# Kernel optimization log

Measured on AMD Instinct MI355X. Metric: run time of the kernel, lower is better.

The kernel has to match this reference:

```python
import jax, jax.numpy as jnp
import numpy as np

D_MODEL = 1024
BATCH = 8
SEQ = 2048
LN_EPS = 1e-5


def setup_inputs() -> dict:
    key = jax.random.key(0)
    ks = jax.random.split(key, 8)
    scale = 0.1 / np.sqrt(D_MODEL)
    x = jax.random.normal(ks[0], (BATCH, SEQ, D_MODEL), dtype=jnp.float32)
    return {
        "x": x,
        "ln_w": jnp.ones((D_MODEL,), jnp.float32),
        "ln_b": jnp.zeros((D_MODEL,), jnp.float32),
        # layer_idx=0, n_layers=4 -> ratio_1 = 1.0 (init), perturb slightly for a non-trivial mix
        "tmk": jnp.ones((D_MODEL,), jnp.float32) * 0.9,
        "tmv": jnp.ones((D_MODEL,), jnp.float32) * 0.9,
        "tmr": jnp.ones((D_MODEL,), jnp.float32) * 0.9,
        "decay_w": jnp.full((D_MODEL,), -0.5, jnp.float32)
        + 0.1 * jax.random.normal(ks[1], (D_MODEL,), jnp.float32),
        "Wk": scale * jax.random.normal(ks[2], (D_MODEL, D_MODEL), jnp.float32),
        "Wv": scale * jax.random.normal(ks[3], (D_MODEL, D_MODEL), jnp.float32),
        "Wr": scale * jax.random.normal(ks[4], (D_MODEL, D_MODEL), jnp.float32),
        "Wo": scale * jax.random.normal(ks[5], (D_MODEL, D_MODEL), jnp.float32),
    }


def _layernorm(z, w, b):
    m = jnp.mean(z, axis=-1, keepdims=True)
    v = jnp.mean(jnp.square(z - m), axis=-1, keepdims=True)
    return (z - m) * jax.lax.rsqrt(v + LN_EPS) * w + b


def reference(x, ln_w, ln_b, tmk, tmv, tmr, decay_w, Wk, Wv, Wr, Wo):
    # x: (B, T, D)
    xn = _layernorm(x, ln_w, ln_b)
    # prev_x at t=0 is zeros (not LN of zeros), afterwards LN(x_{t-1})
    prev = jnp.pad(xn[:, :-1, :], ((0, 0), (1, 0), (0, 0)))
    xk = xn * tmk + prev * (1.0 - tmk)
    xv = xn * tmv + prev * (1.0 - tmv)
    xr = xn * tmr + prev * (1.0 - tmr)
    k = jnp.einsum("btd,ed->bte", xk, Wk)
    v = jnp.einsum("btd,ed->bte", xv, Wv)
    r = jax.nn.sigmoid(jnp.einsum("btd,ed->bte", xr, Wr))
    decay = jax.nn.sigmoid(decay_w)  # (D,)

    kv = (k * v).swapaxes(0, 1)  # (T, B, D) time-major for scan

    def step(S, kv_t):
        S_new = decay * S + kv_t
        return S_new, S_new

    S0 = jnp.zeros((x.shape[0], x.shape[2]), x.dtype)
    final_S, S_seq = jax.lax.scan(step, S0, kv)
    S_seq = S_seq.swapaxes(0, 1)  # (B, T, D)

    out = x + r * jnp.einsum("btd,ed->bte", S_seq, Wo)
    return out, final_S, S_seq
```

## Files before the change

kernel.cpp:

```cpp
#include <hip/hip_runtime.h>
#include <cstdint>

#define D_MODEL 1024
#define SEQ 2048
#define BATCH 8
#define M_TOTAL (BATCH*SEQ)
#define NC 64
#define CL (SEQ/NC)

typedef float f32x4 __attribute__((ext_vector_type(4)));
typedef short bf16x8 __attribute__((ext_vector_type(8)));
typedef unsigned short u16x4 __attribute__((ext_vector_type(4)));

__device__ __forceinline__ float b2f(unsigned short s){
  union { float f; unsigned u; } z; z.u = ((unsigned)s) << 16; return z.f;
}
__device__ __forceinline__ unsigned short f2b(float f){
  union { float f; unsigned u; } z; z.f = f;
  unsigned u = z.u;
  u += 0x7fffu + ((u >> 16) & 1u);
  return (unsigned short)(u >> 16);
}
__device__ __forceinline__ float sigmoidf_(float v){
  return 1.0f / (1.0f + __expf(-v));
}
__device__ __forceinline__ void gld_lds16(const void* g, void* l){
  __builtin_amdgcn_global_load_lds((const __attribute__((address_space(1))) unsigned int*)g,
                                   (__attribute__((address_space(3))) unsigned int*)l,
                                   16, 0, 0);
}

__device__ __forceinline__ void swz256(int bid, int& m0, int& n0){
  int xcd = bid & 7;
  int loc = bid >> 3;
  int wg  = xcd*32 + loc;
  m0 = (wg >> 2) * 256;
  n0 = (wg & 3) * 256;
}

__global__ __launch_bounds__(256) void wconv_kernel(const float* __restrict__ W0, const float* __restrict__ W1,
                                                    const float* __restrict__ W2, const float* __restrict__ W3,
                                                    unsigned short* __restrict__ WC){
  int mat = blockIdx.y;
  const float* src = (mat==0) ? W0 : (mat==1) ? W1 : (mat==2) ? W2 : W3;
  size_t i = ((size_t)blockIdx.x*256 + threadIdx.x)*4;
  f32x4 v = *(const f32x4*)(src + i);
  u16x4 o; o[0]=f2b(v[0]); o[1]=f2b(v[1]); o[2]=f2b(v[2]); o[3]=f2b(v[3]);
  *(u16x4*)(WC + (size_t)mat*1048576 + i) = o;
}

__global__ __launch_bounds__(256) void lnmix_kernel(const float* __restrict__ x,
                                                    const float* __restrict__ lnw, const float* __restrict__ lnb,
                                                    const float* __restrict__ tmk, const float* __restrict__ tmv,
                                                    const float* __restrict__ tmr,
                                                    unsigned short* __restrict__ XK, unsigned short* __restrict__ XV,
                                                    unsigned short* __restrict__ XR){
  int m = blockIdx.x;
  int tid = threadIdx.x;
  bool first = (m & (SEQ-1)) == 0;
  size_t base = (size_t)m*D_MODEL + tid*4;
  f32x4 xc = *(const f32x4*)(x + base);
  f32x4 xp = {0.f,0.f,0.f,0.f};
  if (!first) xp = *(const f32x4*)(x + base - D_MODEL);

  float c1 = xc[0]+xc[1]+xc[2]+xc[3];
  float c2 = xc[0]*xc[0]+xc[1]*xc[1]+xc[2]*xc[2]+xc[3]*xc[3];
  float p1 = xp[0]+xp[1]+xp[2]+xp[3];
  float p2 = xp[0]*xp[0]+xp[1]*xp[1]+xp[2]*xp[2]+xp[3]*xp[3];
  #pragma unroll
  for (int off = 32; off > 0; off >>= 1){
    c1 += __shfl_xor(c1, off); c2 += __shfl_xor(c2, off);
    p1 += __shfl_xor(p1, off); p2 += __shfl_xor(p2, off);
  }
  __shared__ float rc1[4], rc2[4], rp1[4], rp2[4];
  int w = tid >> 6, lane = tid & 63;
  if (lane == 0){ rc1[w]=c1; rc2[w]=c2; rp1[w]=p1; rp2[w]=p2; }
  __syncthreads();
  c1 = rc1[0]+rc1[1]+rc1[2]+rc1[3];
  c2 = rc2[0]+rc2[1]+rc2[2]+rc2[3];
  p1 = rp1[0]+rp1[1]+rp1[2]+rp1[3];
  p2 = rp2[0]+rp2[1]+rp2[2]+rp2[3];
  float mC = c1*(1.0f/1024.0f), vC = c2*(1.0f/1024.0f)-mC*mC, rC = rsqrtf(vC+1e-5f);
  float mP = p1*(1.0f/1024.0f), vP = p2*(1.0f/1024.0f)-mP*mP, rP = rsqrtf(vP+1e-5f);

  f32x4 wv = *(const f32x4*)(lnw + tid*4);
  f32x4 bv = *(const f32x4*)(lnb + tid*4);
  f32x4 k4 = *(const f32x4*)(tmk + tid*4);
  f32x4 v4 = *(const f32x4*)(tmv + tid*4);
  f32x4 r4 = *(const f32x4*)(tmr + tid*4);
  u16x4 ok, ov, orr;
  #pragma unroll
  for (int j=0;j<4;j++){
    float nc = (xc[j]-mC)*rC*wv[j] + bv[j];
    float np = first ? 0.f : (xp[j]-mP)*rP*wv[j] + bv[j];
    ok[j]  = f2b(np + k4[j]*(nc-np));
    ov[j]  = f2b(np + v4[j]*(nc-np));
    orr[j] = f2b(np + r4[j]*(nc-np));
  }
  *(u16x4*)(XK + base) = ok;
  *(u16x4*)(XV + base) = ov;
  *(u16x4*)(XR + base) = orr;
}

__device__ __forceinline__ void gemm256_core(const unsigned short* __restrict__ A,
                                             const unsigned short* __restrict__ W,
                                             int m0, int n0, int tid,
                                             unsigned short* As, unsigned short* Bs,
                                             f32x4 (&acc)[8][4]){
  int wid = tid >> 6, lane = tid & 63;
  int wm = wid >> 2, wn = wid & 3;
  int fr = lane & 15, fg = lane >> 4;

  int offAg[4], offBg[4], offL[4];
  #pragma unroll
  for (int it = 0; it < 4; ++it){
    int chunk = it*512 + tid;
    int row = chunk >> 3;
    int cg = (chunk & 7) ^ (row & 7);
    offAg[it] = (m0+row)*D_MODEL + cg*8;
    offBg[it] = (n0+row)*D_MODEL + cg*8;
    offL[it]  = chunk*8;
  }

  #define STAGE256(bsel, kt) { \
    _Pragma("unroll") \
    for (int it = 0; it < 4; ++it){ \
      gld_lds16(A + offAg[it] + (kt)*64, &As[(bsel)*16384 + offL[it]]); \
      gld_lds16(W + offBg[it] + (kt)*64, &Bs[(bsel)*16384 + offL[it]]); \
    } }

  STAGE256(0, 0);
  for (int kt = 0; kt < 16; ++kt){
    int cur = kt & 1;
    asm volatile("s_waitcnt vmcnt(0)" ::: "memory");
    __builtin_amdgcn_s_barrier();
    if (kt < 15) STAGE256(cur^1, kt+1);
    const unsigned short* Ab = &As[cur*16384];
    const unsigned short* Bb = &Bs[cur*16384];
    #pragma unroll
    for (int ks = 0; ks < 2; ++ks){
      bf16x8 a[8], b[4];
      #pragma unroll
      for (int mi=0; mi<8; ++mi){
        int r = wm*128 + mi*16 + fr;
        a[mi] = *(const bf16x8*)(&Ab[r*64 + (((ks*4+fg) ^ (r&7))<<3)]);
      }
      #pragma unroll
      for (int ni=0; ni<4; ++ni){
        int r = wn*64 + ni*16 + fr;
        b[ni] = *(const bf16x8*)(&Bb[r*64 + (((ks*4+fg) ^ (r&7))<<3)]);
      }
      __builtin_amdgcn_s_setprio(1);
      #pragma unroll
      for (int mi=0; mi<8; ++mi)
        #pragma unroll
        for (int ni=0; ni<4; ++ni)
          acc[mi][ni] = __builtin_amdgcn_mfma_f32_16x16x32_bf16(a[mi], b[ni], acc[mi][ni], 0, 0, 0);
      __builtin_amdgcn_s_setprio(0);
      __builtin_amdgcn_s_barrier();
    }
  }
  #undef STAGE256
}

__global__ __launch_bounds__(512) void gemm_mix3_kernel(const unsigned short* __restrict__ XK,
                                                        const unsigned short* __restrict__ XV,
                                                        const unsigned short* __restrict__ XR,
                                                        const unsigned short* __restrict__ WC,
                                                        unsigned short* __restrict__ KB,
                                                        unsigned short* __restrict__ VB,
                                                        unsigned short* __restrict__ RB){
  __shared__ alignas(16) unsigned short As[2*16384];
  __shared__ alignas(16) unsigned short Bs[2*16384];
  int m0, n0; swz256(blockIdx.x, m0, n0);
  int z = blockIdx.z;
  int tid = threadIdx.x;
  const unsigned short* A = (z==0) ? XK : (z==1) ? XV : XR;
  const unsigned short* W = WC + (size_t)z*1048576;
  unsigned short* O       = (z==0) ? KB : (z==1) ? VB : RB;

  f32x4 acc[8][4];
  #pragma unroll
  for (int i=0;i<8;i++)
    #pragma unroll
    for (int j=0;j<4;j++){ acc[i][j][0]=0.f; acc[i][j][1]=0.f; acc[i][j][2]=0.f; acc[i][j][3]=0.f; }

  gemm256_core(A, W, m0, n0, tid, As, Bs, acc);

  int wid = tid >> 6, lane = tid & 63;
  int wm = wid >> 2, wn = wid & 3;
  int fr = lane & 15, fg = lane >> 4;
  #pragma unroll
  for (int mi=0; mi<8; ++mi){
    #pragma unroll
    for (int ni=0; ni<4; ++ni){
      int c = n0 + wn*64 + ni*16 + fr;
      #pragma unroll
      for (int j=0; j<4; ++j){
        int r = m0 + wm*128 + mi*16 + fg*4 + j;
        size_t idx = (size_t)r*D_MODEL + c;
        float val = acc[mi][ni][j];
        if (z == 2) val = sigmoidf_(val);
        O[idx] = f2b(val);
      }
    }
  }
}

__global__ __launch_bounds__(512) void gemm_out_kernel(const unsigned short* __restrict__ Sb,
                                                       const unsigned short* __restrict__ Wo,
                                                       const float* __restrict__ x,
                                                       const unsigned short* __restrict__ RB,
                                                       float* __restrict__ out){
  __shared__ alignas(16) unsigned short As[2*16384];
  __shared__ alignas(16) unsigned short Bs[2*16384];
  int m0, n0; swz256(blockIdx.x, m0, n0);
  int tid = threadIdx.x;

  f32x4 acc[8][4];
  #pragma unroll
  for (int i=0;i<8;i++)
    #pragma unroll
    for (int j=0;j<4;j++){ acc[i][j][0]=0.f; acc[i][j][1]=0.f; acc[i][j][2]=0.f; acc[i][j][3]=0.f; }

  gemm256_core(Sb, Wo, m0, n0, tid, As, Bs, acc);

  int wid = tid >> 6, lane = tid & 63;
  int wm = wid >> 2, wn = wid & 3;
  int fr = lane & 15, fg = lane >> 4;
  #pragma unroll
  for (int mi=0; mi<8; ++mi){
    #pragma unroll
    for (int ni=0; ni<4; ++ni){
      int c = n0 + wn*64 + ni*16 + fr;
      #pragma unroll
      for (int j=0; j<4; ++j){
        int r = m0 + wm*128 + mi*16 + fg*4 + j;
        size_t idx = (size_t)r*D_MODEL + c;
        float rr = b2f(RB[idx]);
        out[idx] = x[idx] + rr * acc[mi][ni][j];
      }
    }
  }
}

__global__ __launch_bounds__(256) void scan_p1_kernel(const unsigned short* __restrict__ kb,
                                                      const unsigned short* __restrict__ vb,
                                                      const float* __restrict__ dw,
                                                      float* __restrict__ carr){
  int bc = blockIdx.x;
  int b = bc >> 6, c = bc & (NC-1);
  int d0 = threadIdx.x * 4;
  float dx = sigmoidf_(dw[d0+0]);
  float dy = sigmoidf_(dw[d0+1]);
  float dz = sigmoidf_(dw[d0+2]);
  float dwv = sigmoidf_(dw[d0+3]);
  float Sx=0.f, Sy=0.f, Sz=0.f, Sw=0.f;
  size_t base = ((size_t)(b*SEQ + c*CL))*D_MODEL + d0;
  for (int i=0;i<CL;i++){
    u16x4 k4 = *(const u16x4*)(kb + base);
    u16x4 v4 = *(const u16x4*)(vb + base);
    Sx = dx*Sx + b2f(k4[0])*b2f(v4[0]);
    Sy = dy*Sy + b2f(k4[1])*b2f(v4[1]);
    Sz = dz*Sz + b2f(k4[2])*b2f(v4[2]);
    Sw = dwv*Sw + b2f(k4[3])*b2f(v4[3]);
    base += D_MODEL;
  }
  f32x4 o; o[0]=Sx; o[1]=Sy; o[2]=Sz; o[3]=Sw;
  *(f32x4*)(carr + (size_t)bc*D_MODEL + d0) = o;
}

__global__ __launch_bounds__(256) void scan_p2_kernel(const float* __restrict__ dw, float* __restrict__ carr){
  int gid = blockIdx.x*256 + threadIdx.x;
  int b = gid >> 10, d = gid & (D_MODEL-1);
  float dec = sigmoidf_(dw[d]);
  float dL = dec;
  #pragma unroll
  for (int i=0;i<5;i++) dL *= dL;
  float S = 0.f;
  for (int c=0;c<NC;c++){
    size_t idx = ((size_t)(b*NC + c))*D_MODEL + d;
    float cr = carr[idx];
    carr[idx] = S;
    S = dL*S + cr;
  }
}

__global__ __launch_bounds__(256) void scan_p3_kernel(const unsigned short* __restrict__ kb,
                                                      unsigned short* vsb,
                                                      const float* __restrict__ dw,
                                                      const float* __restrict__ cin,
                                                      float* __restrict__ sseq,
                                                      float* __restrict__ finalS){
  int bc = blockIdx.x;
  int b = bc >> 6, c = bc & (NC-1);
  int d0 = threadIdx.x * 4;
  float dx = sigmoidf_(dw[d0+0]);
  float dy = sigmoidf_(dw[d0+1]);
  float dz = sigmoidf_(dw[d0+2]);
  float dwv = sigmoidf_(dw[d0+3]);
  f32x4 S = *(const f32x4*)(cin + (size_t)bc*D_MODEL + d0);
  size_t base = ((size_t)(b*SEQ + c*CL))*D_MODEL + d0;
  for (int i=0;i<CL;i++){
    u16x4 k4 = *(const u16x4*)(kb + base);
    u16x4 v4 = *(const u16x4*)(vsb + base);
    S[0] = dx*S[0] + b2f(k4[0])*b2f(v4[0]);
    S[1] = dy*S[1] + b2f(k4[1])*b2f(v4[1]);
    S[2] = dz*S[2] + b2f(k4[2])*b2f(v4[2]);
    S[3] = dwv*S[3] + b2f(k4[3])*b2f(v4[3]);
    *(f32x4*)(sseq + base) = S;
    u16x4 s4; s4[0]=f2b(S[0]); s4[1]=f2b(S[1]); s4[2]=f2b(S[2]); s4[3]=f2b(S[3]);
    *(u16x4*)(vsb + base) = s4;
    base += D_MODEL;
  }
  if (c == NC-1)
    *(f32x4*)(finalS + (size_t)b*D_MODEL + d0) = S;
}

extern "C" void kernel_launch(void* const* d_in, const int* in_sizes, int n_in,
                              void* d_out, int out_size, void* d_ws, size_t ws_size,
                              hipStream_t stream){
  const float* x   = (const float*)d_in[0];
  const float* lnw = (const float*)d_in[1];
  const float* lnb = (const float*)d_in[2];
  const float* tmk = (const float*)d_in[3];
  const float* tmv = (const float*)d_in[4];
  const float* tmr = (const float*)d_in[5];
  const float* dw  = (const float*)d_in[6];
  const float* Wk  = (const float*)d_in[7];
  const float* Wv  = (const float*)d_in[8];
  const float* Wr  = (const float*)d_in[9];
  const float* Wo  = (const float*)d_in[10];

  float* out    = (float*)d_out;
  float* finalS = out + (size_t)M_TOTAL*D_MODEL;
  float* sseq   = finalS + (size_t)BATCH*D_MODEL;

  unsigned short* XK = (unsigned short*)d_out;
  unsigned short* XV = (unsigned short*)((char*)d_out + 33554432);
  unsigned short* XR = (unsigned short*)sseq;

  char* w = (char*)d_ws;
  unsigned short* WC   = (unsigned short*)(w + 0);
  unsigned short* VSB  = (unsigned short*)(w + 8388608);
  unsigned short* KB   = (unsigned short*)(w + 41943040);
  unsigned short* RB   = (unsigned short*)(w + 75497472);
  float*          CARR = (float*)(w + 109051904);

  wconv_kernel<<<dim3(1024,4), 256, 0, stream>>>(Wk, Wv, Wr, Wo, WC);
  lnmix_kernel<<<M_TOTAL, 256, 0, stream>>>(x, lnw, lnb, tmk, tmv, tmr, XK, XV, XR);

  gemm_mix3_kernel<<<dim3(256,1,3), 512, 0, stream>>>(XK, XV, XR, WC, KB, VSB, RB);

  scan_p1_kernel<<<BATCH*NC, 256, 0, stream>>>(KB, VSB, dw, CARR);
  scan_p2_kernel<<<32, 256, 0, stream>>>(dw, CARR);
  scan_p3_kernel<<<BATCH*NC, 256, 0, stream>>>(KB, VSB, dw, CARR, sseq, finalS);

  gemm_out_kernel<<<256, 512, 0, stream>>>(VSB, WC + (size_t)3*1048576, x, RB, out);
}
```

Measured before the change: 287.8 us.

## Use 256x128 GEMM tiles with triple-buffered LDS and deeper prefetch

Shrinks the GEMM tile from 256x256 to 256x128, which doubles the grid to 512 blocks per matrix (1536 for the fused k/v/r launch), and updates the XCD swizzle to match. The K loop moves from double to triple buffering with a prefetch distance of two. It waits with a partial vmcnt and uses one barrier per iteration instead of two. The aim is more blocks to fill the CUs, fewer accumulator registers, and more load latency hidden. The cost is more LDS (144KB per block), lower arithmetic intensity per tile, and more A re-reads.

```diff
diff --git a/kernel.cpp b/kernel.cpp
--- a/kernel.cpp
+++ b/kernel.cpp
@@ -30,12 +30,12 @@
                                    16, 0, 0);
 }
 
-__device__ __forceinline__ void swz256(int bid, int& m0, int& n0){
+__device__ __forceinline__ void swz_mn(int bid, int& m0, int& n0){
   int xcd = bid & 7;
   int loc = bid >> 3;
-  int wg  = xcd*32 + loc;
-  m0 = (wg >> 2) * 256;
-  n0 = (wg & 3) * 256;
+  int wg  = xcd*64 + loc;
+  m0 = (wg >> 3) * 256;
+  n0 = (wg & 7) * 128;
 }
 
 __global__ __launch_bounds__(256) void wconv_kernel(const float* __restrict__ W0, const float* __restrict__ W1,
@@ -106,61 +106,85 @@
                                              const unsigned short* __restrict__ W,
                                              int m0, int n0, int tid,
                                              unsigned short* As, unsigned short* Bs,
-                                             f32x4 (&acc)[8][4]){
+                                             f32x4 (&acc)[8][2]){
   int wid = tid >> 6, lane = tid & 63;
   int wm = wid >> 2, wn = wid & 3;
   int fr = lane & 15, fg = lane >> 4;
 
-  int offAg[4], offBg[4], offL[4];
+  int offAg[4], offBg[2], offLA[4], offLB[2];
   #pragma unroll
   for (int it = 0; it < 4; ++it){
     int chunk = it*512 + tid;
     int row = chunk >> 3;
     int cg = (chunk & 7) ^ (row & 7);
     offAg[it] = (m0+row)*D_MODEL + cg*8;
+    offLA[it] = chunk*8;
+  }
+  #pragma unroll
+  for (int it = 0; it < 2; ++it){
+    int chunk = it*512 + tid;
+    int row = chunk >> 3;
+    int cg = (chunk & 7) ^ (row & 7);
     offBg[it] = (n0+row)*D_MODEL + cg*8;
-    offL[it]  = chunk*8;
-  }
-
-  #define STAGE256(bsel, kt) { \
+    offLB[it] = chunk*8;
+  }
+
+  #define STAGE(bsel, kt) { \
     _Pragma("unroll") \
-    for (int it = 0; it < 4; ++it){ \
-      gld_lds16(A + offAg[it] + (kt)*64, &As[(bsel)*16384 + offL[it]]); \
-      gld_lds16(W + offBg[it] + (kt)*64, &Bs[(bsel)*16384 + offL[it]]); \
-    } }
-
-  STAGE256(0, 0);
-  for (int kt = 0; kt < 16; ++kt){
-    int cur = kt & 1;
-    asm volatile("s_waitcnt vmcnt(0)" ::: "memory");
+    for (int it = 0; it < 4; ++it) \
+      gld_lds16(A + offAg[it] + (kt)*64, &As[(bsel)*16384 + offLA[it]]); \
+    _Pragma("unroll") \
+    for (int it = 0; it < 2; ++it) \
+      gld_lds16(W + offBg[it] + (kt)*64, &Bs[(bsel)*8192 + offLB[it]]); \
+  }
+
+  #define COMPUTE(bsel) { \
+    const unsigned short* Ab = &As[(bsel)*16384]; \
+    const unsigned short* Bb = &Bs[(bsel)*8192]; \
+    _Pragma("unroll") \
+    for (int ks = 0; ks < 2; ++ks){ \
+      bf16x8 a[8], b[2]; \
+      _Pragma("unroll") \
+      for (int mi=0; mi<8; ++mi){ \
+        int r = wm*128 + mi*16 + fr; \
+        a[mi] = *(const bf16x8*)(&Ab[r*64 + (((ks*4+fg) ^ (r&7))<<3)]); \
+      } \
+      _Pragma("unroll") \
+      for (int ni=0; ni<2; ++ni){ \
+        int r = wn*32 + ni*16 + fr; \
+        b[ni] = *(const bf16x8*)(&Bb[r*64 + (((ks*4+fg) ^ (r&7))<<3)]); \
+      } \
+      __builtin_amdgcn_s_setprio(1); \
+      _Pragma("unroll") \
+      for (int mi=0; mi<8; ++mi) \
+        _Pragma("unroll") \
+        for (int ni=0; ni<2; ++ni) \
+          acc[mi][ni] = __builtin_amdgcn_mfma_f32_16x16x32_bf16(a[mi], b[ni], acc[mi][ni], 0, 0, 0); \
+      __builtin_amdgcn_s_setprio(0); \
+    } \
+  }
+
+  STAGE(0, 0);
+  STAGE(1, 1);
+  int cur = 0;
+  #pragma unroll 1
+  for (int kt = 0; kt < 15; ++kt){
+    asm volatile("s_waitcnt vmcnt(6)" ::: "memory");
     __builtin_amdgcn_s_barrier();
-    if (kt < 15) STAGE256(cur^1, kt+1);
-    const unsigned short* Ab = &As[cur*16384];
-    const unsigned short* Bb = &Bs[cur*16384];
-    #pragma unroll
-    for (int ks = 0; ks < 2; ++ks){
-      bf16x8 a[8], b[4];
-      #pragma unroll
-      for (int mi=0; mi<8; ++mi){
-        int r = wm*128 + mi*16 + fr;
-        a[mi] = *(const bf16x8*)(&Ab[r*64 + (((ks*4+fg) ^ (r&7))<<3)]);
-      }
-      #pragma unroll
-      for (int ni=0; ni<4; ++ni){
-        int r = wn*64 + ni*16 + fr;
-        b[ni] = *(const bf16x8*)(&Bb[r*64 + (((ks*4+fg) ^ (r&7))<<3)]);
-      }
-      __builtin_amdgcn_s_setprio(1);
-      #pragma unroll
-      for (int mi=0; mi<8; ++mi)
-        #pragma unroll
-        for (int ni=0; ni<4; ++ni)
-          acc[mi][ni] = __builtin_amdgcn_mfma_f32_16x16x32_bf16(a[mi], b[ni], acc[mi][ni], 0, 0, 0);
-      __builtin_amdgcn_s_setprio(0);
-      __builtin_amdgcn_s_barrier();
+    asm volatile("" ::: "memory");
+    if (kt < 14){
+      int nb = cur + 2; if (nb >= 3) nb -= 3;
+      STAGE(nb, kt+2);
     }
-  }
-  #undef STAGE256
+    COMPUTE(cur);
+    cur = (cur == 2) ? 0 : cur + 1;
+  }
+  asm volatile("s_waitcnt vmcnt(0)" ::: "memory");
+  __builtin_amdgcn_s_barrier();
+  asm volatile("" ::: "memory");
+  COMPUTE(cur);
+  #undef STAGE
+  #undef COMPUTE
 }
 
 __global__ __launch_bounds__(512) void gemm_mix3_kernel(const unsigned short* __restrict__ XK,
@@ -170,20 +194,20 @@
                                                         unsigned short* __restrict__ KB,
                                                         unsigned short* __restrict__ VB,
                                                         unsigned short* __restrict__ RB){
-  __shared__ alignas(16) unsigned short As[2*16384];
-  __shared__ alignas(16) unsigned short Bs[2*16384];
-  int m0, n0; swz256(blockIdx.x, m0, n0);
+  __shared__ alignas(16) unsigned short As[3*16384];
+  __shared__ alignas(16) unsigned short Bs[3*8192];
+  int m0, n0; swz_mn(blockIdx.x, m0, n0);
   int z = blockIdx.z;
   int tid = threadIdx.x;
   const unsigned short* A = (z==0) ? XK : (z==1) ? XV : XR;
   const unsigned short* W = WC + (size_t)z*1048576;
   unsigned short* O       = (z==0) ? KB : (z==1) ? VB : RB;
 
-  f32x4 acc[8][4];
+  f32x4 acc[8][2];
   #pragma unroll
   for (int i=0;i<8;i++)
     #pragma unroll
-    for (int j=0;j<4;j++){ acc[i][j][0]=0.f; acc[i][j][1]=0.f; acc[i][j][2]=0.f; acc[i][j][3]=0.f; }
+    for (int j=0;j<2;j++){ acc[i][j][0]=0.f; acc[i][j][1]=0.f; acc[i][j][2]=0.f; acc[i][j][3]=0.f; }
 
   gemm256_core(A, W, m0, n0, tid, As, Bs, acc);
 
@@ -193,8 +217,8 @@
   #pragma unroll
   for (int mi=0; mi<8; ++mi){
     #pragma unroll
-    for (int ni=0; ni<4; ++ni){
-      int c = n0 + wn*64 + ni*16 + fr;
+    for (int ni=0; ni<2; ++ni){
+      int c = n0 + wn*32 + ni*16 + fr;
       #pragma unroll
       for (int j=0; j<4; ++j){
         int r = m0 + wm*128 + mi*16 + fg*4 + j;
@@ -212,16 +236,16 @@
                                                        const float* __restrict__ x,
                                                        const unsigned short* __restrict__ RB,
                                                        float* __restrict__ out){
-  __shared__ alignas(16) unsigned short As[2*16384];
-  __shared__ alignas(16) unsigned short Bs[2*16384];
-  int m0, n0; swz256(blockIdx.x, m0, n0);
+  __shared__ alignas(16) unsigned short As[3*16384];
+  __shared__ alignas(16) unsigned short Bs[3*8192];
+  int m0, n0; swz_mn(blockIdx.x, m0, n0);
   int tid = threadIdx.x;
 
-  f32x4 acc[8][4];
+  f32x4 acc[8][2];
   #pragma unroll
   for (int i=0;i<8;i++)
     #pragma unroll
-    for (int j=0;j<4;j++){ acc[i][j][0]=0.f; acc[i][j][1]=0.f; acc[i][j][2]=0.f; acc[i][j][3]=0.f; }
+    for (int j=0;j<2;j++){ acc[i][j][0]=0.f; acc[i][j][1]=0.f; acc[i][j][2]=0.f; acc[i][j][3]=0.f; }
 
   gemm256_core(Sb, Wo, m0, n0, tid, As, Bs, acc);
 
@@ -231,8 +255,8 @@
   #pragma unroll
   for (int mi=0; mi<8; ++mi){
     #pragma unroll
-    for (int ni=0; ni<4; ++ni){
-      int c = n0 + wn*64 + ni*16 + fr;
+    for (int ni=0; ni<2; ++ni){
+      int c = n0 + wn*32 + ni*16 + fr;
       #pragma unroll
       for (int j=0; j<4; ++j){
         int r = m0 + wm*128 + mi*16 + fg*4 + j;
@@ -350,11 +374,11 @@
   wconv_kernel<<<dim3(1024,4), 256, 0, stream>>>(Wk, Wv, Wr, Wo, WC);
   lnmix_kernel<<<M_TOTAL, 256, 0, stream>>>(x, lnw, lnb, tmk, tmv, tmr, XK, XV, XR);
 
-  gemm_mix3_kernel<<<dim3(256,1,3), 512, 0, stream>>>(XK, XV, XR, WC, KB, VSB, RB);
+  gemm_mix3_kernel<<<dim3(512,1,3), 512, 0, stream>>>(XK, XV, XR, WC, KB, VSB, RB);
 
   scan_p1_kernel<<<BATCH*NC, 256, 0, stream>>>(KB, VSB, dw, CARR);
   scan_p2_kernel<<<32, 256, 0, stream>>>(dw, CARR);
   scan_p3_kernel<<<BATCH*NC, 256, 0, stream>>>(KB, VSB, dw, CARR, sseq, finalS);
 
-  gemm_out_kernel<<<256, 512, 0, stream>>>(VSB, WC + (size_t)3*1048576, x, RB, out);
-}
+  gemm_out_kernel<<<512, 512, 0, stream>>>(VSB, WC + (size_t)3*1048576, x, RB, out);
+}
```

After: 321.1 us. 1.12x slower.

## Restructure 256x256 GEMM main loop into quadrant-phased MFMA with two-ahead prefetch

Applied to the files above, without the earlier changes.

Reworks the inner GEMM loop so each K-tile is processed in four quadrant phases (A-low/B-low, A-low/B-high, A-high/B-high, A-high/B-low). LDS fragment loads are interleaved with MFMA bursts, separated by barriers and lgkmcnt waits. Global-to-LDS staging now issues two tiles ahead and waits with vmcnt(8) instead of vmcnt(0), so global loads overlap more compute. The added barriers and the buffer-reuse timing add synchronisation complexity and raise the risk of a race on the LDS buffers.

```diff
diff --git a/kernel.cpp b/kernel.cpp
--- a/kernel.cpp
+++ b/kernel.cpp
@@ -122,45 +122,110 @@
     offL[it]  = chunk*8;
   }
 
-  #define STAGE256(bsel, kt) { \
+  #define STAGE(bsel, kt_) { \
     _Pragma("unroll") \
     for (int it = 0; it < 4; ++it){ \
-      gld_lds16(A + offAg[it] + (kt)*64, &As[(bsel)*16384 + offL[it]]); \
-      gld_lds16(W + offBg[it] + (kt)*64, &Bs[(bsel)*16384 + offL[it]]); \
+      gld_lds16(A + offAg[it] + (kt_)*64, &As[(bsel)*16384 + offL[it]]); \
+      gld_lds16(W + offBg[it] + (kt_)*64, &Bs[(bsel)*16384 + offL[it]]); \
     } }
 
-  STAGE256(0, 0);
+  STAGE(0, 0);
+  STAGE(1, 1);
+  asm volatile("s_waitcnt vmcnt(8)" ::: "memory");
+  __builtin_amdgcn_s_barrier();
+
+  bf16x8 aL[4][2], aH[4][2], bL[2][2], bH[2][2];
+
+  #pragma unroll 1
   for (int kt = 0; kt < 16; ++kt){
-    int cur = kt & 1;
-    asm volatile("s_waitcnt vmcnt(0)" ::: "memory");
+    const unsigned short* Ab = &As[(kt & 1)*16384];
+    const unsigned short* Bb = &Bs[(kt & 1)*16384];
+
+    #pragma unroll
+    for (int mi=0; mi<4; ++mi)
+      #pragma unroll
+      for (int ks=0; ks<2; ++ks){
+        int r = wm*128 + mi*16 + fr;
+        aL[mi][ks] = *(const bf16x8*)(&Ab[r*64 + (((ks*4+fg)^(r&7))<<3)]);
+      }
+    #pragma unroll
+    for (int ni=0; ni<2; ++ni)
+      #pragma unroll
+      for (int ks=0; ks<2; ++ks){
+        int r = wn*64 + ni*16 + fr;
+        bL[ni][ks] = *(const bf16x8*)(&Bb[r*64 + (((ks*4+fg)^(r&7))<<3)]);
+      }
     __builtin_amdgcn_s_barrier();
-    if (kt < 15) STAGE256(cur^1, kt+1);
-    const unsigned short* Ab = &As[cur*16384];
-    const unsigned short* Bb = &Bs[cur*16384];
-    #pragma unroll
-    for (int ks = 0; ks < 2; ++ks){
-      bf16x8 a[8], b[4];
-      #pragma unroll
-      for (int mi=0; mi<8; ++mi){
-        int r = wm*128 + mi*16 + fr;
-        a[mi] = *(const bf16x8*)(&Ab[r*64 + (((ks*4+fg) ^ (r&7))<<3)]);
-      }
-      #pragma unroll
-      for (int ni=0; ni<4; ++ni){
-        int r = wn*64 + ni*16 + fr;
-        b[ni] = *(const bf16x8*)(&Bb[r*64 + (((ks*4+fg) ^ (r&7))<<3)]);
-      }
-      __builtin_amdgcn_s_setprio(1);
-      #pragma unroll
-      for (int mi=0; mi<8; ++mi)
+    asm volatile("s_waitcnt lgkmcnt(0)" ::: "memory");
+    __builtin_amdgcn_s_setprio(1);
+    #pragma unroll
+    for (int mi=0; mi<4; ++mi)
+      #pragma unroll
+      for (int ni=0; ni<2; ++ni)
         #pragma unroll
-        for (int ni=0; ni<4; ++ni)
-          acc[mi][ni] = __builtin_amdgcn_mfma_f32_16x16x32_bf16(a[mi], b[ni], acc[mi][ni], 0, 0, 0);
-      __builtin_amdgcn_s_setprio(0);
+        for (int ks=0; ks<2; ++ks)
+          acc[mi][ni] = __builtin_amdgcn_mfma_f32_16x16x32_bf16(aL[mi][ks], bL[ni][ks], acc[mi][ni], 0, 0, 0);
+    __builtin_amdgcn_s_setprio(0);
+    __builtin_amdgcn_s_barrier();
+
+    #pragma unroll
+    for (int ni=0; ni<2; ++ni)
+      #pragma unroll
+      for (int ks=0; ks<2; ++ks){
+        int r = wn*64 + (ni+2)*16 + fr;
+        bH[ni][ks] = *(const bf16x8*)(&Bb[r*64 + (((ks*4+fg)^(r&7))<<3)]);
+      }
+    __builtin_amdgcn_s_barrier();
+    asm volatile("s_waitcnt lgkmcnt(0)" ::: "memory");
+    __builtin_amdgcn_s_setprio(1);
+    #pragma unroll
+    for (int mi=0; mi<4; ++mi)
+      #pragma unroll
+      for (int ni=0; ni<2; ++ni)
+        #pragma unroll
+        for (int ks=0; ks<2; ++ks)
+          acc[mi][ni+2] = __builtin_amdgcn_mfma_f32_16x16x32_bf16(aL[mi][ks], bH[ni][ks], acc[mi][ni+2], 0, 0, 0);
+    __builtin_amdgcn_s_setprio(0);
+    __builtin_amdgcn_s_barrier();
+
+    #pragma unroll
+    for (int mi=0; mi<4; ++mi)
+      #pragma unroll
+      for (int ks=0; ks<2; ++ks){
+        int r = wm*128 + (mi+4)*16 + fr;
+        aH[mi][ks] = *(const bf16x8*)(&Ab[r*64 + (((ks*4+fg)^(r&7))<<3)]);
+      }
+    asm volatile("s_waitcnt lgkmcnt(0)" ::: "memory");
+    __builtin_amdgcn_s_barrier();
+    asm volatile("" ::: "memory");
+    __builtin_amdgcn_s_setprio(1);
+    #pragma unroll
+    for (int mi=0; mi<4; ++mi)
+      #pragma unroll
+      for (int ni=0; ni<2; ++ni)
+        #pragma unroll
+        for (int ks=0; ks<2; ++ks)
+          acc[mi+4][ni+2] = __builtin_amdgcn_mfma_f32_16x16x32_bf16(aH[mi][ks], bH[ni][ks], acc[mi+4][ni+2], 0, 0, 0);
+    __builtin_amdgcn_s_setprio(0);
+
+    if (kt < 14) STAGE((kt & 1), kt+2);
+    __builtin_amdgcn_s_setprio(1);
+    #pragma unroll
+    for (int mi=0; mi<4; ++mi)
+      #pragma unroll
+      for (int ni=0; ni<2; ++ni)
+        #pragma unroll
+        for (int ks=0; ks<2; ++ks)
+          acc[mi+4][ni] = __builtin_amdgcn_mfma_f32_16x16x32_bf16(aH[mi][ks], bL[ni][ks], acc[mi+4][ni], 0, 0, 0);
+    __builtin_amdgcn_s_setprio(0);
+    if (kt < 14)      asm volatile("s_waitcnt vmcnt(8)" ::: "memory");
+    else if (kt == 14) asm volatile("s_waitcnt vmcnt(0)" ::: "memory");
+    if (kt < 15){
       __builtin_amdgcn_s_barrier();
+      asm volatile("" ::: "memory");
     }
   }
-  #undef STAGE256
+  #undef STAGE
 }
 
 __global__ __launch_bounds__(512) void gemm_mix3_kernel(const unsigned short* __restrict__ XK,
```

New measurement: 289.0 us. About the same (+0.4%).
